# Kernel tuning notes

Hardware: AMD Instinct MI355X
Metric: run time of the kernel (lower is better)

Reference implementation:

```python
import jax, jax.numpy as jnp
import numpy as np

DIL = 2  # dilation_rate from init_kwargs

def _conv_same(x, w, b, dil=DIL):
    # x: [B,H,W,C], w: [kh,kw,Cin,Cout] (HWIO), 'same' padding with dilation, stride 1
    y = jax.lax.conv_general_dilated(
        x, w, window_strides=(1, 1), padding='SAME',
        rhs_dilation=(dil, dil),
        dimension_numbers=('NHWC', 'HWIO', 'NHWC'))
    return y + b


def setup_inputs() -> dict:
    key = jax.random.key(0)
    ks = jax.random.split(key, 4)
    B, H, W, C = 8, 128, 256, 64
    F, VF, K = 64, 64, 3
    X = jax.random.normal(ks[0], (B, H, W, C), dtype=jnp.float32)
    Wq = jax.random.normal(ks[1], (K, K, C, F), dtype=jnp.float32) * 0.05
    Wk = jax.random.normal(ks[2], (K, K, C, F), dtype=jnp.float32) * 0.05
    Wv = jax.random.normal(ks[3], (K, K, C, VF), dtype=jnp.float32) * 0.05
    bq = jnp.zeros((F,), jnp.float32)
    bk = jnp.zeros((F,), jnp.float32)
    bv = jnp.zeros((VF,), jnp.float32)
    return {"X": X, "Wq": Wq, "bq": bq, "Wk": Wk, "bk": bk, "Wv": Wv, "bv": bv}


def reference(X, Wq, bq, Wk, bk, Wv, bv):
    q = _conv_same(X, Wq, bq)   # [B,H,W,F]
    k = _conv_same(X, Wk, bk)   # [B,H,W,F]
    v = _conv_same(X, Wv, bv)   # [B,H,W,VF]
    # tf.matmul(q, k, transpose_b=True): batch dims [B,H], attend along W. No scaling.
    scores = jnp.einsum('bhqf,bhkf->bhqk', q, k)          # [B,H,W,W]
    attn = jax.nn.softmax(scores, axis=-1)
    return jnp.einsum('bhqk,bhkf->bhqf', attn, v)         # [B,H,W,VF]
```

## Files before the change

### kernel.cpp

```cpp
#include <hip/hip_runtime.h>

#define B_ 8
#define H_ 128
#define W_ 256
#define C_ 64
#define F_ 64

typedef __attribute__((ext_vector_type(8))) short short8;
typedef __attribute__((ext_vector_type(8))) _Float16 half8;
typedef __attribute__((ext_vector_type(4))) float f32x4;

__device__ __forceinline__ unsigned short f2h(float x) {
    _Float16 h = (_Float16)x;
    return __builtin_bit_cast(unsigned short, h);
}

__device__ __forceinline__ f32x4 mfma16(short8 a, short8 b, f32x4 c) {
    return __builtin_amdgcn_mfma_f32_16x16x32_f16(
        __builtin_bit_cast(half8, a), __builtin_bit_cast(half8, b), c, 0, 0, 0);
}

__global__ void wprep_kernel(const float* __restrict__ Wq,
                             const float* __restrict__ Wk,
                             const float* __restrict__ Wv,
                             unsigned short* __restrict__ Wt)
{
    int e = blockIdx.x * 256 + threadIdx.x;
    int c   = e & 63;
    int f   = (e >> 6) % 192;
    int tap = e / 12288;
    const float* src = (f < 64) ? Wq : (f < 128) ? Wk : Wv;
    int ff = f & 63;
    float v = src[(long)tap * 4096 + c * 64 + ff];
    Wt[e] = f2h(v);
}

#define XST 72
#define WST 72

__global__ __launch_bounds__(256, 2) void conv_mfma(
    const float* __restrict__ X, const unsigned short* __restrict__ Wt,
    const float* __restrict__ bq, const float* __restrict__ bk,
    const float* __restrict__ bv,
    unsigned short* __restrict__ Qg, unsigned short* __restrict__ Kg,
    unsigned short* __restrict__ Vtg)
{
    __shared__ __align__(16) unsigned short Xs[260 * XST];
    __shared__ __align__(16) unsigned short Wls[288 * WST];

    const int tid  = threadIdx.x;
    const int wv   = tid >> 6;
    const int lane = tid & 63;
    const int l15  = lane & 15;
    const int g    = lane >> 4;
    const int bx   = blockIdx.x;
    const int bh   = bx >> 1;
    const int half = bx & 1;
    const int b    = bh >> 7;
    const int h    = bh & 127;

    f32x4 acc[4][6];
    #pragma unroll
    for (int mt = 0; mt < 4; ++mt)
        #pragma unroll
        for (int nt = 0; nt < 6; ++nt)
            acc[mt][nt] = (f32x4){0.f, 0.f, 0.f, 0.f};

    for (int kh = 0; kh < 3; ++kh) {
        const int ih = h + 2 * (kh - 1);
        if ((unsigned)ih >= (unsigned)H_) continue;
        const float* Xr = X + ((long)(b * H_ + ih) * W_) * C_;

        __syncthreads();

        for (int e = tid; e < 260 * 16; e += 256) {
            const int row = e >> 4, c4 = e & 15;
            const int w_in = row - 2;
            float4 val = make_float4(0.f, 0.f, 0.f, 0.f);
            if ((unsigned)w_in < (unsigned)W_)
                val = *(const float4*)(Xr + (long)w_in * 64 + c4 * 4);
            uint2 p;
            p.x = (unsigned)f2h(val.x) | ((unsigned)f2h(val.y) << 16);
            p.y = (unsigned)f2h(val.z) | ((unsigned)f2h(val.w) << 16);
            *(uint2*)(Xs + row * XST + c4 * 4) = p;
        }
        for (int e = tid; e < 2304; e += 256) {
            const int c8 = e & 7, f = (e >> 3) % 96, kw = e / 768;
            uint4 d = *(const uint4*)(Wt +
                (((long)(kh * 3 + kw) * 192 + half * 96 + f) * 64 + c8 * 8));
            *(uint4*)(Wls + (kw * 96 + f) * WST + c8 * 8) = d;
        }
        __syncthreads();

        #pragma unroll
        for (int kw = 0; kw < 3; ++kw) {
            short8 bfrag[6][2];
            #pragma unroll
            for (int nt = 0; nt < 6; ++nt)
                #pragma unroll
                for (int kt = 0; kt < 2; ++kt)
                    bfrag[nt][kt] = *(const short8*)(Wls +
                        (kw * 96 + nt * 16 + l15) * WST + (kt * 4 + g) * 8);
            #pragma unroll
            for (int kt = 0; kt < 2; ++kt)
                #pragma unroll
                for (int mt = 0; mt < 4; ++mt) {
                    const int row = wv * 64 + mt * 16 + l15 + 2 * kw;
                    short8 a = *(const short8*)(Xs + row * XST + (kt * 4 + g) * 8);
                    #pragma unroll
                    for (int nt = 0; nt < 6; ++nt)
                        acc[mt][nt] = mfma16(a, bfrag[nt][kt], acc[mt][nt]);
                }
        }
    }

    float bias[6];
    #pragma unroll
    for (int nt = 0; nt < 6; ++nt) {
        const int fp = half * 96 + nt * 16 + l15;
        bias[nt] = (fp < 64) ? bq[fp] : (fp < 128) ? bk[fp - 64] : bv[fp - 128];
    }
    #pragma unroll
    for (int mt = 0; mt < 4; ++mt) {
        const int wrow = wv * 64 + mt * 16 + 4 * g;
        #pragma unroll
        for (int nt = 0; nt < 6; ++nt) {
            const int fp = half * 96 + nt * 16 + l15;
            if (fp < 128) {
                unsigned short* dst = (fp < 64) ? Qg : Kg;
                const int f = fp & 63;
                #pragma unroll
                for (int r = 0; r < 4; ++r)
                    dst[((long)bh * 256 + wrow + r) * 64 + f] =
                        f2h(acc[mt][nt][r] + bias[nt]);
            } else {
                const int f = fp - 128;
                uint2 p;
                p.x = (unsigned)f2h(acc[mt][nt][0] + bias[nt]) |
                      ((unsigned)f2h(acc[mt][nt][1] + bias[nt]) << 16);
                p.y = (unsigned)f2h(acc[mt][nt][2] + bias[nt]) |
                      ((unsigned)f2h(acc[mt][nt][3] + bias[nt]) << 16);
                *(uint2*)(Vtg + ((long)bh * 64 + f) * 256 + wrow) = p;
            }
        }
    }
}

#define QST 72
#define PST 40

__global__ __launch_bounds__(256, 2) void attn_mfma(
    const unsigned short* __restrict__ Qg, const unsigned short* __restrict__ Kg,
    const unsigned short* __restrict__ Vtg, float* __restrict__ Out)
{
    __shared__ __align__(16) unsigned short Qs[256 * QST];
    __shared__ __align__(16) unsigned short Ks[32 * QST];
    __shared__ __align__(16) unsigned short Vts[64 * PST];
    __shared__ __align__(16) unsigned short Ps[4][64 * PST];

    const int tid  = threadIdx.x;
    const int wv   = tid >> 6;
    const int lane = tid & 63;
    const int l15  = lane & 15;
    const int g    = lane >> 4;
    const long bh  = blockIdx.x;

    const unsigned short* Qb = Qg + bh * 256 * 64;
    #pragma unroll
    for (int it = 0; it < 8; ++it) {
        const int row = it * 32 + (tid >> 3), s = tid & 7;
        uint4 d = *(const uint4*)(Qb + row * 64 + s * 8);
        *(uint4*)(Qs + row * QST + s * 8) = d;
    }
    __syncthreads();

    short8 qf[4][2];
    #pragma unroll
    for (int mt = 0; mt < 4; ++mt)
        #pragma unroll
        for (int kt = 0; kt < 2; ++kt)
            qf[mt][kt] = *(const short8*)(Qs +
                (wv * 64 + mt * 16 + l15) * QST + (kt * 4 + g) * 8);

    f32x4 po[4][4];
    float mrun[4][4], lrun[4][4];
    #pragma unroll
    for (int mt = 0; mt < 4; ++mt) {
        #pragma unroll
        for (int nt = 0; nt < 4; ++nt) po[mt][nt] = (f32x4){0.f,0.f,0.f,0.f};
        #pragma unroll
        for (int r = 0; r < 4; ++r) { mrun[mt][r] = -3.0e38f; lrun[mt][r] = 0.f; }
    }

    unsigned short* Pw = &Ps[wv][0];

    for (int t0 = 0; t0 < 256; t0 += 32) {
        __syncthreads();
        {
            const int u = tid >> 3, s = tid & 7;
            uint4 d = *(const uint4*)(Kg + (bh * 256 + t0 + u) * 64 + s * 8);
            *(uint4*)(Ks + u * QST + s * 8) = d;
        }
        {
            const int f = tid >> 2, c4 = tid & 3;
            uint4 d = *(const uint4*)(Vtg + (bh * 64 + f) * 256 + t0 + c4 * 8);
            *(uint4*)(Vts + f * PST + c4 * 8) = d;
        }
        __syncthreads();

        f32x4 s[4][2];
        #pragma unroll
        for (int mt = 0; mt < 4; ++mt)
            #pragma unroll
            for (int nt = 0; nt < 2; ++nt) s[mt][nt] = (f32x4){0.f,0.f,0.f,0.f};
        #pragma unroll
        for (int kt = 0; kt < 2; ++kt) {
            #pragma unroll
            for (int nt = 0; nt < 2; ++nt) {
                const int kv = nt * 16 + l15;
                short8 kb = *(const short8*)(Ks + kv * QST + (kt * 4 + g) * 8);
                #pragma unroll
                for (int mt = 0; mt < 4; ++mt)
                    s[mt][nt] = mfma16(qf[mt][kt], kb, s[mt][nt]);
            }
        }

        #pragma unroll
        for (int mt = 0; mt < 4; ++mt) {
            #pragma unroll
            for (int r = 0; r < 4; ++r) {
                float t = fmaxf(s[mt][0][r], s[mt][1][r]);
                t = fmaxf(t, __shfl_xor(t, 1));
                t = fmaxf(t, __shfl_xor(t, 2));
                t = fmaxf(t, __shfl_xor(t, 4));
                t = fmaxf(t, __shfl_xor(t, 8));
                const float mo = mrun[mt][r];
                const float mn = fmaxf(mo, t);
                const float al = __expf(mo - mn);
                mrun[mt][r] = mn;
                const float p0 = __expf(s[mt][0][r] - mn);
                const float p1 = __expf(s[mt][1][r] - mn);
                float ss = p0 + p1;
                ss += __shfl_xor(ss, 1);
                ss += __shfl_xor(ss, 2);
                ss += __shfl_xor(ss, 4);
                ss += __shfl_xor(ss, 8);
                lrun[mt][r] = lrun[mt][r] * al + ss;
                #pragma unroll
                for (int nf = 0; nf < 4; ++nf) po[mt][nf][r] *= al;
                const int wrow = mt * 16 + 4 * g + r;
                Pw[wrow * PST + l15]      = f2h(p0);
                Pw[wrow * PST + 16 + l15] = f2h(p1);
            }
        }

        short8 vb[4];
        #pragma unroll
        for (int nf = 0; nf < 4; ++nf)
            vb[nf] = *(const short8*)(Vts + (nf * 16 + l15) * PST + g * 8);
        #pragma unroll
        for (int mt = 0; mt < 4; ++mt) {
            short8 pa = *(const short8*)(Pw + (mt * 16 + l15) * PST + g * 8);
            #pragma unroll
            for (int nf = 0; nf < 4; ++nf)
                po[mt][nf] = mfma16(pa, vb[nf], po[mt][nf]);
        }
    }

    #pragma unroll
    for (int mt = 0; mt < 4; ++mt) {
        #pragma unroll
        for (int r = 0; r < 4; ++r) {
            const float inv = 1.0f / lrun[mt][r];
            const long wrow = bh * 256 + wv * 64 + mt * 16 + 4 * g + r;
            #pragma unroll
            for (int nf = 0; nf < 4; ++nf)
                Out[wrow * 64 + nf * 16 + l15] = po[mt][nf][r] * inv;
        }
    }
}

extern "C" void kernel_launch(void* const* d_in, const int* in_sizes, int n_in,
                              void* d_out, int out_size, void* d_ws, size_t ws_size,
                              hipStream_t stream) {
    const float* X  = (const float*)d_in[0];
    const float* Wq = (const float*)d_in[1];
    const float* bq = (const float*)d_in[2];
    const float* Wk = (const float*)d_in[3];
    const float* bk = (const float*)d_in[4];
    const float* Wv = (const float*)d_in[5];
    const float* bv = (const float*)d_in[6];
    float* out = (float*)d_out;

    const size_t NE = (size_t)B_ * H_ * W_ * F_;
    unsigned short* q  = (unsigned short*)d_ws;
    unsigned short* k  = q + NE;
    unsigned short* vt = k + NE;
    unsigned short* wt = vt + NE;

    wprep_kernel<<<432, 256, 0, stream>>>(Wq, Wk, Wv, wt);
    conv_mfma<<<B_ * H_ * 2, 256, 0, stream>>>(X, wt, bq, bk, bv, q, k, vt);
    attn_mfma<<<B_ * H_, 256, 0, stream>>>(q, k, vt, out);
}
```

Before: 344.3 us.

## Split conv channel staging, double-buffer attention K/V tiles, lazy softmax rescale

The conv kernel now stages input and weights in two 32-channel halves, which shrinks LDS use and raises the occupancy target to 3 blocks per CU. The attention kernel loads Q fragments straight from global memory and processes 64-key tiles. K/V tiles are double-buffered so the next tile's loads overlap compute, and only one barrier is kept per tile. It skips the online-softmax rescale when the running max grows by no more than 8, and computes the row sums with an MFMA against a ones vector instead of shuffle reductions. The trade-offs are more barriers in the conv kernel, and a thresholded rescale that can let unnormalised fp16 probabilities grow to about e^8.

After: 336.2 us. 1.02x faster.

```diff
diff --git a/kernel.cpp b/kernel.cpp
--- a/kernel.cpp
+++ b/kernel.cpp
@@ -35,10 +35,10 @@
     Wt[e] = f2h(v);
 }
 
-#define XST 72
-#define WST 72
-
-__global__ __launch_bounds__(256, 2) void conv_mfma(
+#define XST 36
+#define WST 36
+
+__global__ __launch_bounds__(256, 3) void conv_mfma(
     const float* __restrict__ X, const unsigned short* __restrict__ Wt,
     const float* __restrict__ bq, const float* __restrict__ bk,
     const float* __restrict__ bv,
@@ -71,46 +71,45 @@
         if ((unsigned)ih >= (unsigned)H_) continue;
         const float* Xr = X + ((long)(b * H_ + ih) * W_) * C_;
 
-        __syncthreads();
-
-        for (int e = tid; e < 260 * 16; e += 256) {
-            const int row = e >> 4, c4 = e & 15;
-            const int w_in = row - 2;
-            float4 val = make_float4(0.f, 0.f, 0.f, 0.f);
-            if ((unsigned)w_in < (unsigned)W_)
-                val = *(const float4*)(Xr + (long)w_in * 64 + c4 * 4);
-            uint2 p;
-            p.x = (unsigned)f2h(val.x) | ((unsigned)f2h(val.y) << 16);
-            p.y = (unsigned)f2h(val.z) | ((unsigned)f2h(val.w) << 16);
-            *(uint2*)(Xs + row * XST + c4 * 4) = p;
-        }
-        for (int e = tid; e < 2304; e += 256) {
-            const int c8 = e & 7, f = (e >> 3) % 96, kw = e / 768;
-            uint4 d = *(const uint4*)(Wt +
-                (((long)(kh * 3 + kw) * 192 + half * 96 + f) * 64 + c8 * 8));
-            *(uint4*)(Wls + (kw * 96 + f) * WST + c8 * 8) = d;
-        }
-        __syncthreads();
-
-        #pragma unroll
-        for (int kw = 0; kw < 3; ++kw) {
-            short8 bfrag[6][2];
-            #pragma unroll
-            for (int nt = 0; nt < 6; ++nt)
-                #pragma unroll
-                for (int kt = 0; kt < 2; ++kt)
-                    bfrag[nt][kt] = *(const short8*)(Wls +
-                        (kw * 96 + nt * 16 + l15) * WST + (kt * 4 + g) * 8);
-            #pragma unroll
-            for (int kt = 0; kt < 2; ++kt)
+        for (int cc = 0; cc < 2; ++cc) {
+            const int c0 = cc * 32;
+            __syncthreads();
+
+            for (int e = tid; e < 260 * 8; e += 256) {
+                const int row = e >> 3, c4 = e & 7;
+                const int w_in = row - 2;
+                float4 val = make_float4(0.f, 0.f, 0.f, 0.f);
+                if ((unsigned)w_in < (unsigned)W_)
+                    val = *(const float4*)(Xr + (long)w_in * 64 + c0 + c4 * 4);
+                uint2 p;
+                p.x = (unsigned)f2h(val.x) | ((unsigned)f2h(val.y) << 16);
+                p.y = (unsigned)f2h(val.z) | ((unsigned)f2h(val.w) << 16);
+                *(uint2*)(Xs + row * XST + c4 * 4) = p;
+            }
+            for (int e = tid; e < 1152; e += 256) {
+                const int c8 = e & 3, f = (e >> 2) % 96, kw = e / 384;
+                uint4 d = *(const uint4*)(Wt +
+                    (((long)(kh * 3 + kw) * 192 + half * 96 + f) * 64 + c0 + c8 * 8));
+                *(uint4*)(Wls + (kw * 96 + f) * WST + c8 * 8) = d;
+            }
+            __syncthreads();
+
+            #pragma unroll
+            for (int kw = 0; kw < 3; ++kw) {
+                short8 bfrag[6];
+                #pragma unroll
+                for (int nt = 0; nt < 6; ++nt)
+                    bfrag[nt] = *(const short8*)(Wls +
+                        (kw * 96 + nt * 16 + l15) * WST + g * 8);
                 #pragma unroll
                 for (int mt = 0; mt < 4; ++mt) {
                     const int row = wv * 64 + mt * 16 + l15 + 2 * kw;
-                    short8 a = *(const short8*)(Xs + row * XST + (kt * 4 + g) * 8);
+                    short8 a = *(const short8*)(Xs + row * XST + g * 8);
                     #pragma unroll
                     for (int nt = 0; nt < 6; ++nt)
-                        acc[mt][nt] = mfma16(a, bfrag[nt][kt], acc[mt][nt]);
+                        acc[mt][nt] = mfma16(a, bfrag[nt], acc[mt][nt]);
                 }
+            }
         }
     }
 
@@ -146,16 +145,15 @@
     }
 }
 
-#define QST 72
-#define PST 40
+#define KST 72
+#define PST 72
 
 __global__ __launch_bounds__(256, 2) void attn_mfma(
     const unsigned short* __restrict__ Qg, const unsigned short* __restrict__ Kg,
     const unsigned short* __restrict__ Vtg, float* __restrict__ Out)
 {
-    __shared__ __align__(16) unsigned short Qs[256 * QST];
-    __shared__ __align__(16) unsigned short Ks[32 * QST];
-    __shared__ __align__(16) unsigned short Vts[64 * PST];
+    __shared__ __align__(16) unsigned short Ks[2][64 * KST];
+    __shared__ __align__(16) unsigned short Vts[2][64 * KST];
     __shared__ __align__(16) unsigned short Ps[4][64 * PST];
 
     const int tid  = threadIdx.x;
@@ -165,105 +163,131 @@
     const int g    = lane >> 4;
     const long bh  = blockIdx.x;
 
-    const unsigned short* Qb = Qg + bh * 256 * 64;
-    #pragma unroll
-    for (int it = 0; it < 8; ++it) {
-        const int row = it * 32 + (tid >> 3), s = tid & 7;
-        uint4 d = *(const uint4*)(Qb + row * 64 + s * 8);
-        *(uint4*)(Qs + row * QST + s * 8) = d;
-    }
-    __syncthreads();
-
     short8 qf[4][2];
     #pragma unroll
     for (int mt = 0; mt < 4; ++mt)
         #pragma unroll
         for (int kt = 0; kt < 2; ++kt)
-            qf[mt][kt] = *(const short8*)(Qs +
-                (wv * 64 + mt * 16 + l15) * QST + (kt * 4 + g) * 8);
-
-    f32x4 po[4][4];
-    float mrun[4][4], lrun[4][4];
+            qf[mt][kt] = *(const short8*)(Qg +
+                (bh * 256 + wv * 64 + mt * 16 + l15) * 64 + (kt * 4 + g) * 8);
+
+    const int srow = tid >> 2, sch = (tid & 3) * 16;
+
+    {
+        const unsigned short* kp = Kg + (bh * 256 + srow) * 64 + sch;
+        const unsigned short* vp = Vtg + (bh * 64 + srow) * 256 + sch;
+        *(uint4*)(Ks[0] + srow * KST + sch)     = *(const uint4*)(kp);
+        *(uint4*)(Ks[0] + srow * KST + sch + 8) = *(const uint4*)(kp + 8);
+        *(uint4*)(Vts[0] + srow * KST + sch)     = *(const uint4*)(vp);
+        *(uint4*)(Vts[0] + srow * KST + sch + 8) = *(const uint4*)(vp + 8);
+    }
+
+    f32x4 po[4][4], lacc[4];
+    float mrun[4][4];
     #pragma unroll
     for (int mt = 0; mt < 4; ++mt) {
         #pragma unroll
         for (int nt = 0; nt < 4; ++nt) po[mt][nt] = (f32x4){0.f,0.f,0.f,0.f};
-        #pragma unroll
-        for (int r = 0; r < 4; ++r) { mrun[mt][r] = -3.0e38f; lrun[mt][r] = 0.f; }
-    }
+        lacc[mt] = (f32x4){0.f,0.f,0.f,0.f};
+        #pragma unroll
+        for (int r = 0; r < 4; ++r) mrun[mt][r] = -3.0e38f;
+    }
+
+    short8 ones;
+    #pragma unroll
+    for (int i = 0; i < 8; ++i) ones[i] = (short)0x3C00;
 
     unsigned short* Pw = &Ps[wv][0];
 
-    for (int t0 = 0; t0 < 256; t0 += 32) {
+    for (int t = 0; t < 4; ++t) {
         __syncthreads();
-        {
-            const int u = tid >> 3, s = tid & 7;
-            uint4 d = *(const uint4*)(Kg + (bh * 256 + t0 + u) * 64 + s * 8);
-            *(uint4*)(Ks + u * QST + s * 8) = d;
-        }
-        {
-            const int f = tid >> 2, c4 = tid & 3;
-            uint4 d = *(const uint4*)(Vtg + (bh * 64 + f) * 256 + t0 + c4 * 8);
-            *(uint4*)(Vts + f * PST + c4 * 8) = d;
-        }
-        __syncthreads();
-
-        f32x4 s[4][2];
+        const int cur = t & 1;
+        if (t < 3) {
+            const int nx = cur ^ 1, t0 = (t + 1) * 64;
+            const unsigned short* kp = Kg + (bh * 256 + t0 + srow) * 64 + sch;
+            const unsigned short* vp = Vtg + (bh * 64 + srow) * 256 + t0 + sch;
+            *(uint4*)(Ks[nx] + srow * KST + sch)     = *(const uint4*)(kp);
+            *(uint4*)(Ks[nx] + srow * KST + sch + 8) = *(const uint4*)(kp + 8);
+            *(uint4*)(Vts[nx] + srow * KST + sch)     = *(const uint4*)(vp);
+            *(uint4*)(Vts[nx] + srow * KST + sch + 8) = *(const uint4*)(vp + 8);
+        }
+
+        f32x4 s[4][4];
         #pragma unroll
         for (int mt = 0; mt < 4; ++mt)
             #pragma unroll
-            for (int nt = 0; nt < 2; ++nt) s[mt][nt] = (f32x4){0.f,0.f,0.f,0.f};
-        #pragma unroll
-        for (int kt = 0; kt < 2; ++kt) {
-            #pragma unroll
-            for (int nt = 0; nt < 2; ++nt) {
-                const int kv = nt * 16 + l15;
-                short8 kb = *(const short8*)(Ks + kv * QST + (kt * 4 + g) * 8);
+            for (int nt = 0; nt < 4; ++nt) s[mt][nt] = (f32x4){0.f,0.f,0.f,0.f};
+        #pragma unroll
+        for (int kt = 0; kt < 2; ++kt)
+            #pragma unroll
+            for (int nt = 0; nt < 4; ++nt) {
+                short8 kb = *(const short8*)(Ks[cur] +
+                    (nt * 16 + l15) * KST + (kt * 4 + g) * 8);
                 #pragma unroll
                 for (int mt = 0; mt < 4; ++mt)
                     s[mt][nt] = mfma16(qf[mt][kt], kb, s[mt][nt]);
             }
-        }
 
         #pragma unroll
         for (int mt = 0; mt < 4; ++mt) {
+            float tm[4];
             #pragma unroll
             for (int r = 0; r < 4; ++r) {
-                float t = fmaxf(s[mt][0][r], s[mt][1][r]);
-                t = fmaxf(t, __shfl_xor(t, 1));
-                t = fmaxf(t, __shfl_xor(t, 2));
-                t = fmaxf(t, __shfl_xor(t, 4));
-                t = fmaxf(t, __shfl_xor(t, 8));
-                const float mo = mrun[mt][r];
-                const float mn = fmaxf(mo, t);
-                const float al = __expf(mo - mn);
-                mrun[mt][r] = mn;
-                const float p0 = __expf(s[mt][0][r] - mn);
-                const float p1 = __expf(s[mt][1][r] - mn);
-                float ss = p0 + p1;
-                ss += __shfl_xor(ss, 1);
-                ss += __shfl_xor(ss, 2);
-                ss += __shfl_xor(ss, 4);
-                ss += __shfl_xor(ss, 8);
-                lrun[mt][r] = lrun[mt][r] * al + ss;
-                #pragma unroll
-                for (int nf = 0; nf < 4; ++nf) po[mt][nf][r] *= al;
-                const int wrow = mt * 16 + 4 * g + r;
-                Pw[wrow * PST + l15]      = f2h(p0);
-                Pw[wrow * PST + 16 + l15] = f2h(p1);
-            }
-        }
-
-        short8 vb[4];
-        #pragma unroll
-        for (int nf = 0; nf < 4; ++nf)
-            vb[nf] = *(const short8*)(Vts + (nf * 16 + l15) * PST + g * 8);
-        #pragma unroll
-        for (int mt = 0; mt < 4; ++mt) {
-            short8 pa = *(const short8*)(Pw + (mt * 16 + l15) * PST + g * 8);
+                float a0 = fmaxf(s[mt][0][r], s[mt][1][r]);
+                float a1 = fmaxf(s[mt][2][r], s[mt][3][r]);
+                float t0 = fmaxf(a0, a1);
+                t0 = fmaxf(t0, __shfl_xor(t0, 1));
+                t0 = fmaxf(t0, __shfl_xor(t0, 2));
+                t0 = fmaxf(t0, __shfl_xor(t0, 4));
+                t0 = fmaxf(t0, __shfl_xor(t0, 8));
+                tm[r] = t0;
+            }
+            float worst = tm[0] - mrun[mt][0];
+            #pragma unroll
+            for (int r = 1; r < 4; ++r) worst = fmaxf(worst, tm[r] - mrun[mt][r]);
+            if (__all(worst <= 8.f)) {
+                #pragma unroll
+                for (int r = 0; r < 4; ++r) {
+                    const float mo = mrun[mt][r];
+                    const int wrow = mt * 16 + 4 * g + r;
+                    #pragma unroll
+                    for (int nt = 0; nt < 4; ++nt)
+                        Pw[wrow * PST + nt * 16 + l15] = f2h(__expf(s[mt][nt][r] - mo));
+                }
+            } else {
+                #pragma unroll
+                for (int r = 0; r < 4; ++r) {
+                    const float mo = mrun[mt][r];
+                    const float mn = fmaxf(mo, tm[r]);
+                    const float al = __expf(mo - mn);
+                    mrun[mt][r] = mn;
+                    lacc[mt][r] *= al;
+                    #pragma unroll
+                    for (int nf = 0; nf < 4; ++nf) po[mt][nf][r] *= al;
+                    const int wrow = mt * 16 + 4 * g + r;
+                    #pragma unroll
+                    for (int nt = 0; nt < 4; ++nt)
+                        Pw[wrow * PST + nt * 16 + l15] = f2h(__expf(s[mt][nt][r] - mn));
+                }
+            }
+        }
+
+        #pragma unroll
+        for (int kt = 0; kt < 2; ++kt) {
+            short8 vb[4];
             #pragma unroll
             for (int nf = 0; nf < 4; ++nf)
-                po[mt][nf] = mfma16(pa, vb[nf], po[mt][nf]);
+                vb[nf] = *(const short8*)(Vts[cur] +
+                    (nf * 16 + l15) * KST + (kt * 4 + g) * 8);
+            #pragma unroll
+            for (int mt = 0; mt < 4; ++mt) {
+                short8 pa = *(const short8*)(Pw +
+                    (mt * 16 + l15) * PST + (kt * 4 + g) * 8);
+                #pragma unroll
+                for (int nf = 0; nf < 4; ++nf)
+                    po[mt][nf] = mfma16(pa, vb[nf], po[mt][nf]);
+                lacc[mt] = mfma16(pa, ones, lacc[mt]);
+            }
         }
     }
 
@@ -271,7 +295,7 @@
     for (int mt = 0; mt < 4; ++mt) {
         #pragma unroll
         for (int r = 0; r < 4; ++r) {
-            const float inv = 1.0f / lrun[mt][r];
+            const float inv = 1.0f / lacc[mt][r];
             const long wrow = bh * 256 + wv * 64 + mt * 16 + 4 * g + r;
             #pragma unroll
             for (int nf = 0; nf < 4; ++nf)
```
